# Kernel tuning notes

Hardware: AMD Instinct MI355X
Metric: run time of the kernel (lower is better)

Reference implementation:

```python
import jax, jax.numpy as jnp
import numpy as np

NH = 50000; NO = 50000; E = 500000; D = 256; L = 8; B = 512; C = 117


def setup_inputs() -> dict:
    key = jax.random.key(0)
    ks = jax.random.split(key, 32)
    s = 0.05
    inp = {
        'x_human': jax.random.normal(ks[0], (NH, D), jnp.float32),
        'x_object': jax.random.normal(ks[1], (NO, D), jnp.float32),
        'edge_index_ho': jax.random.randint(ks[2], (2, E), 0, NH),
        'edge_index_oh': jax.random.randint(ks[3], (2, E), 0, NO),
        'edge_attr_ho': jax.random.normal(ks[4], (E, 2), jnp.float32),
        'edge_attr_oh': jax.random.normal(ks[5], (E, 2), jnp.float32),
        'hbatch': jnp.sort(jax.random.randint(ks[6], (NH,), 0, B)),
        'obatch': jnp.sort(jax.random.randint(ks[7], (NO,), 0, B)),
    }
    # GATConv params per relation, stacked over L layers
    names = ['Wsrc', 'Wdst', 'asrc', 'adst', 'Wedge', 'aedge', 'bias']
    shapes = [(L, D, D), (L, D, D), (L, D), (L, D), (L, 2, D), (L, D), (L, D)]
    i = 8
    for rel in ['ho', 'oh']:
        for n, sh in zip(names, shapes):
            inp[f'{n}_{rel}'] = jax.random.normal(ks[i], sh, jnp.float32) * s
            i += 1
    inp['W_emlp'] = jax.random.normal(ks[i], (2, 32), jnp.float32) * s
    inp['b_emlp'] = jnp.zeros((32,), jnp.float32)
    inp['W_p1'] = jax.random.normal(ks[i + 1], (2 * D + 32, C), jnp.float32) * s
    inp['b_p1'] = jnp.zeros((C,), jnp.float32)
    inp['W_p2'] = jax.random.normal(ks[i + 2], (2 * D + 32, C), jnp.float32) * s
    inp['b_p2'] = jnp.zeros((C,), jnp.float32)
    return inp


def _gat(x_src, x_dst, ei, ea, Wsrc, Wdst, asrc, adst, Wedge, aedge, bias, num_dst):
    # PyG GATConv (heads=1, edge_dim=2, add_self_loops=False)
    h_src = x_src @ Wsrc                       # [Ns, D]
    h_dst = x_dst @ Wdst                       # [Nd, D]
    src, dst = ei[0], ei[1]
    a_s = h_src @ asrc                         # [Ns]
    a_d = h_dst @ adst                         # [Nd]
    a_e = (ea @ Wedge) @ aedge                 # [E]
    logit = jax.nn.leaky_relu(a_s[src] + a_d[dst] + a_e, 0.2)
    m = jax.ops.segment_max(logit, dst, num_segments=num_dst)
    ex = jnp.exp(logit - m[dst])
    denom = jax.ops.segment_sum(ex, dst, num_segments=num_dst)
    alpha = ex / denom[dst]                    # segment softmax over dst
    out = jax.ops.segment_sum(h_src[src] * alpha[:, None], dst, num_segments=num_dst)
    return out + bias


def _seg_mean(x, seg, num):
    s = jax.ops.segment_sum(x, seg, num_segments=num)
    cnt = jax.ops.segment_sum(jnp.ones((x.shape[0],), x.dtype), seg, num_segments=num)
    return s / jnp.maximum(cnt, 1.0)[:, None]


def reference(x_human, x_object, edge_index_ho, edge_index_oh, edge_attr_ho,
              edge_attr_oh, hbatch, obatch,
              Wsrc_ho, Wdst_ho, asrc_ho, adst_ho, Wedge_ho, aedge_ho, bias_ho,
              Wsrc_oh, Wdst_oh, asrc_oh, adst_oh, Wedge_oh, aedge_oh, bias_oh,
              W_emlp, b_emlp, W_p1, b_p1, W_p2, b_p2):
    xh, xo = x_human, x_object
    ph, po = None, None
    for l in range(L):
        nxo = _gat(xh, xo, edge_index_ho, edge_attr_ho, Wsrc_ho[l], Wdst_ho[l],
                   asrc_ho[l], adst_ho[l], Wedge_ho[l], aedge_ho[l], bias_ho[l], NO)
        nxh = _gat(xo, xh, edge_index_oh, edge_attr_oh, Wsrc_oh[l], Wdst_oh[l],
                   asrc_oh[l], adst_oh[l], Wedge_oh[l], aedge_oh[l], bias_oh[l], NH)
        nxh = jax.nn.relu(nxh)
        nxo = jax.nn.relu(nxo)
        if ph is not None:
            nxh = nxh + ph
            nxo = nxo + po
        ph, po = nxh, nxo
        xh, xo = nxh, nxo
    hpool = _seg_mean(xh, hbatch, B)           # [B, D]
    opool = _seg_mean(xo, obatch, B)           # [B, D]
    ea = jax.nn.relu(edge_attr_ho @ W_emlp + b_emlp)  # [E, 32]
    edge_batch = hbatch[edge_index_ho[0]]
    epool = _seg_mean(ea, edge_batch, B)       # [B, 32]
    graph_emb = jnp.concatenate([hpool, opool, epool], axis=-1)  # [B, 544]
    l1 = jax.nn.softmax(graph_emb @ W_p1 + b_p1, axis=1)
    l2 = jax.nn.softmax(graph_emb @ W_p2 + b_p2, axis=1)
    return jnp.stack((l1, l2), axis=1)         # [B, 2, C]
```

## Files before the change

### kernel.cpp

```cpp
#include <hip/hip_runtime.h>
#include <math.h>


#define NNODE 50000
#define EDG   500000
#define DIM   256
#define LAY   8
#define BB    512
#define CC    117
#define EMBD  544
#define SCB   49

typedef short bf16x8 __attribute__((ext_vector_type(8)));
typedef float f32x4  __attribute__((ext_vector_type(4)));

static __device__ __forceinline__ float lrelu(float x){ return x >= 0.f ? x : 0.2f*x; }
static __device__ __forceinline__ unsigned short f2b(float f){
  unsigned int u = __float_as_uint(f);
  unsigned int r = (u + 0x7fffu + ((u >> 16) & 1u)) >> 16;
  return (unsigned short)r;
}
static __device__ __forceinline__ float b2f(unsigned short u){
  return __uint_as_float(((unsigned int)u) << 16);
}

__global__ void vcompute_k(const float* __restrict__ Wsho, const float* __restrict__ Wdho,
                           const float* __restrict__ asho, const float* __restrict__ adho,
                           const float* __restrict__ Wsoh, const float* __restrict__ Wdoh,
                           const float* __restrict__ asoh, const float* __restrict__ adoh,
                           float* __restrict__ vbuf){
  int gid = blockIdx.x*blockDim.x + threadIdx.x;
  int wv = gid >> 6, lane = gid & 63;
  if (wv >= 32*DIM) return;
  int p = wv >> 8, k = wv & 255;
  int which = p & 1, rel = (p>>1)&1, l = p>>2;
  const float* W; const float* a;
  if (rel==0){ W = which? Wdho : Wsho; a = which? adho : asho; }
  else       { W = which? Wdoh : Wsoh; a = which? adoh : asoh; }
  W += (size_t)l*DIM*DIM; a += (size_t)l*DIM;
  const float4* w4 = (const float4*)(W + (size_t)k*DIM);
  const float4* a4 = (const float4*)a;
  float4 wv4 = w4[lane], av4 = a4[lane];
  float s = wv4.x*av4.x + wv4.y*av4.y + wv4.z*av4.z + wv4.w*av4.w;
  for (int off=32; off; off>>=1) s += __shfl_xor(s, off);
  if (lane==0) vbuf[(size_t)p*DIM + k] = s;
}

__global__ void wecompute_k(const float* __restrict__ Weho, const float* __restrict__ aeho,
                            const float* __restrict__ Weoh, const float* __restrict__ aeoh,
                            float* __restrict__ webuf){
  int blk = blockIdx.x;
  int rel = blk & 1, l = blk >> 1;
  const float* We = rel? Weoh : Weho;
  const float* ae = rel? aeoh : aeho;
  int lane = threadIdx.x;
  const float4* w0 = (const float4*)(We + (size_t)l*2*DIM);
  const float4* w1 = (const float4*)(We + (size_t)l*2*DIM + DIM);
  const float4* a4 = (const float4*)(ae + (size_t)l*DIM);
  float4 av = a4[lane], x0 = w0[lane], x1 = w1[lane];
  float s0 = x0.x*av.x + x0.y*av.y + x0.z*av.z + x0.w*av.w;
  float s1 = x1.x*av.x + x1.y*av.y + x1.z*av.z + x1.w*av.w;
  for (int off=32; off; off>>=1){ s0 += __shfl_xor(s0, off); s1 += __shfl_xor(s1, off); }
  if (lane==0){ webuf[blk*2] = s0; webuf[blk*2+1] = s1; }
}

__global__ void hist3_k(const int* __restrict__ ei_ho, const int* __restrict__ ei_oh,
                        int* __restrict__ cnt_ho, int* __restrict__ cnt_oh,
                        int* __restrict__ cnt_src){
  int e = blockIdx.x*blockDim.x + threadIdx.x;
  if (e >= EDG) return;
  int y = blockIdx.y;
  if (y == 0)      atomicAdd(&cnt_ho[ei_ho[EDG + e]], 1);
  else if (y == 1) atomicAdd(&cnt_oh[ei_oh[EDG + e]], 1);
  else             atomicAdd(&cnt_src[ei_ho[e]], 1);
}

__global__ void scanA_k(const int* __restrict__ c0, const int* __restrict__ c1,
                        const int* __restrict__ c2, int* __restrict__ bsum){
  __shared__ int sh[256];
  int y = blockIdx.y, b = blockIdx.x, t = threadIdx.x;
  const int* cnt = (y==0)? c0 : (y==1)? c1 : c2;
  int idx = b*1024 + t*4;
  int s = 0;
  if (idx + 3 < NNODE){
    int4 v = *(const int4*)(cnt + idx);
    s = v.x + v.y + v.z + v.w;
  } else {
    for (int j=0;j<4;j++) if (idx+j < NNODE) s += cnt[idx+j];
  }
  sh[t] = s; __syncthreads();
  for (int off=128; off; off>>=1){ if (t<off) sh[t] += sh[t+off]; __syncthreads(); }
  if (t==0) bsum[y*SCB + b] = sh[0];
}

__global__ void scanB_k(int* __restrict__ bsum, int* __restrict__ boff,
                        int* __restrict__ rp0, int* __restrict__ rp1, int* __restrict__ rp2){
  int t = threadIdx.x;
  if (t >= 3) return;
  int run = 0;
  for (int i=0;i<SCB;i++){ boff[t*SCB+i] = run; run += bsum[t*SCB+i]; }
  int* rp = (t==0)? rp0 : (t==1)? rp1 : rp2;
  rp[NNODE] = run;
}

__global__ void scanC_k(const int* __restrict__ c0, const int* __restrict__ c1,
                        const int* __restrict__ c2, const int* __restrict__ boff,
                        int* __restrict__ rp0, int* __restrict__ rp1, int* __restrict__ rp2){
  __shared__ int sh[256];
  int y = blockIdx.y, b = blockIdx.x, t = threadIdx.x;
  const int* cnt = (y==0)? c0 : (y==1)? c1 : c2;
  int* rp = (y==0)? rp0 : (y==1)? rp1 : rp2;
  int idx = b*1024 + t*4;
  int c[4] = {0,0,0,0};
  if (idx + 3 < NNODE){
    int4 v = *(const int4*)(cnt + idx);
    c[0]=v.x; c[1]=v.y; c[2]=v.z; c[3]=v.w;
  } else {
    for (int j=0;j<4;j++) if (idx+j < NNODE) c[j] = cnt[idx+j];
  }
  int mysum = c[0]+c[1]+c[2]+c[3];
  sh[t] = mysum; __syncthreads();
  for (int off=1; off<256; off<<=1){
    int v = (t>=off) ? sh[t-off] : 0;
    __syncthreads();
    sh[t] += v;
    __syncthreads();
  }
  int base = boff[y*SCB + b] + (sh[t] - mysum);
  int run = 0;
  for (int j=0;j<4;j++){
    if (idx+j < NNODE) rp[idx+j] = base + run;
    run += c[j];
  }
}

__global__ void scatter_k(const int* __restrict__ ei, const float* __restrict__ ea,
                          const int* __restrict__ rowptr, int* __restrict__ cursor,
                          int* __restrict__ srcs, float2* __restrict__ eaperm){
  int e = blockIdx.x*blockDim.x + threadIdx.x;
  if (e >= EDG) return;
  int d = ei[EDG + e];
  int pos = rowptr[d] + atomicAdd(&cursor[d], 1);
  srcs[pos] = ei[e];
  eaperm[pos] = make_float2(ea[2*e], ea[2*e+1]);
}

__global__ void scatter_src_k(const int* __restrict__ ei, const float* __restrict__ ea,
                              const int* __restrict__ rowptr, int* __restrict__ cursor,
                              float2* __restrict__ eaperm){
  int e = blockIdx.x*blockDim.x + threadIdx.x;
  if (e >= EDG) return;
  int s = ei[e];
  int pos = rowptr[s] + atomicAdd(&cursor[s], 1);
  eaperm[pos] = make_float2(ea[2*e], ea[2*e+1]);
}

__global__ void xconv_k(const float* __restrict__ in, unsigned short* __restrict__ out, int n4){
  int i = blockIdx.x*blockDim.x + threadIdx.x;
  if (i >= n4) return;
  float4 v = ((const float4*)in)[i];
  ushort4 o; o.x=f2b(v.x); o.y=f2b(v.y); o.z=f2b(v.z); o.w=f2b(v.w);
  ((ushort4*)out)[i] = o;
}

__global__ void wtconv_k(const float* __restrict__ Who, const float* __restrict__ Woh,
                         unsigned short* __restrict__ Wt){
  int gid = blockIdx.x*blockDim.x + threadIdx.x;
  int rel = gid >> 19;
  int rem = gid & ((1<<19)-1);
  int l = rem >> 16;
  int idx = rem & 65535;
  int n = idx >> 8, k = idx & 255;
  const float* W = rel ? Woh : Who;
  Wt[gid] = f2b(W[(size_t)l*65536 + (size_t)k*256 + n]);
}

__global__ __launch_bounds__(256) void gemmb_k(const unsigned short* __restrict__ A,
                                               const unsigned short* __restrict__ Bt,
                                               unsigned short* __restrict__ H, int M){
  __shared__ __align__(16) unsigned short As[4096];
  __shared__ __align__(16) unsigned short Bs[4096];
  int tid = threadIdx.x;
  int col0 = blockIdx.x * 128;
  int row0 = blockIdx.y * 128;
  int w = tid >> 6, lane = tid & 63;
  int q = lane >> 4, ml = lane & 15;
  f32x4 acc[2][8];
  #pragma unroll
  for (int i=0;i<2;i++)
    #pragma unroll
    for (int j=0;j<8;j++) acc[i][j] = (f32x4){0.f,0.f,0.f,0.f};
  int srow = tid >> 2;
  int sq   = tid & 3;
  for (int k0 = 0; k0 < 256; k0 += 32){
    #pragma unroll
    for (int p = 0; p < 2; ++p){
      int row = p*64 + srow;
      int gr = row0 + row;
      uint4 av = make_uint4(0,0,0,0);
      if (gr < M) av = *(const uint4*)(A + (size_t)gr*256 + k0 + sq*8);
      *(uint4*)&As[((((row>>4)*4) + sq)*16 + (row&15))*8] = av;
      int gc = col0 + row;
      uint4 bv = *(const uint4*)(Bt + (size_t)gc*256 + k0 + sq*8);
      *(uint4*)&Bs[((((row>>4)*4) + sq)*16 + (row&15))*8] = bv;
    }
    __syncthreads();
    bf16x8 a0 = *(const bf16x8*)&As[(((2*w+0)*4 + q)*16 + ml)*8];
    bf16x8 a1 = *(const bf16x8*)&As[(((2*w+1)*4 + q)*16 + ml)*8];
    #pragma unroll
    for (int nf = 0; nf < 8; ++nf){
      bf16x8 b = *(const bf16x8*)&Bs[((nf*4 + q)*16 + ml)*8];
      acc[0][nf] = __builtin_amdgcn_mfma_f32_16x16x32_bf16(a0, b, acc[0][nf], 0,0,0);
      acc[1][nf] = __builtin_amdgcn_mfma_f32_16x16x32_bf16(a1, b, acc[1][nf], 0,0,0);
    }
    __syncthreads();
  }
  #pragma unroll
  for (int mf = 0; mf < 2; ++mf){
    #pragma unroll
    for (int r = 0; r < 4; ++r){
      int gr = row0 + 32*w + 16*mf + q*4 + r;
      if (gr < M){
        #pragma unroll
        for (int nf = 0; nf < 8; ++nf)
          H[(size_t)gr*256 + col0 + nf*16 + ml] = f2b(acc[mf][nf][r]);
      }
    }
  }
}

__global__ void dgemv_k(const float* __restrict__ X, const float* __restrict__ v1,
                        const float* __restrict__ v2, float* __restrict__ o1,
                        float* __restrict__ o2){
  int gid = blockIdx.x*blockDim.x + threadIdx.x;
  int w = gid >> 6, lane = gid & 63;
  if (w >= NNODE) return;
  const float4* x4 = (const float4*)(X + (size_t)w*DIM);
  float4 xv = x4[lane];
  float4 a = ((const float4*)v1)[lane];
  float4 b = ((const float4*)v2)[lane];
  float s1 = xv.x*a.x + xv.y*a.y + xv.z*a.z + xv.w*a.w;
  float s2 = xv.x*b.x + xv.y*b.y + xv.z*b.z + xv.w*b.w;
  for (int off=32; off; off>>=1){ s1 += __shfl_xor(s1, off); s2 += __shfl_xor(s2, off); }
  if (lane==0){ o1[w] = s1; o2[w] = s2; }
}

__global__ void attn_k(const int* __restrict__ rowptr, const int* __restrict__ srcs,
                       const float2* __restrict__ eaperm, const float* __restrict__ a_s,
                       const float* __restrict__ a_d,
                       const float* __restrict__ wep, const unsigned short* __restrict__ hs,
                       const float* __restrict__ bias, const unsigned short* __restrict__ xprev,
                       unsigned short* __restrict__ xnext,
                       const float* __restrict__ vsn, const float* __restrict__ vdn,
                       float* __restrict__ asn, float* __restrict__ adn,
                       int hasRes, int doNext){
  int gid = blockIdx.x*blockDim.x + threadIdx.x;
  int w = gid >> 6, lane = gid & 63;
  if (w >= NNODE) return;
  int st = rowptr[w], en = rowptr[w+1];
  int deg = en - st;
  float w0 = wep[0], w1 = wep[1];
  float adv = a_d[w];
  float ax=0.f, ay=0.f, az=0.f, aw=0.f;
  const ushort4* h4 = (const ushort4*)hs;
  if (deg > 0 && deg <= 64){
    int sreg = 0; float lg = -INFINITY;
    if (lane < deg){
      sreg = srcs[st + lane];
      float2 ev = eaperm[st + lane];
      lg = lrelu(a_s[sreg] + adv + ev.x*w0 + ev.y*w1);
    }
    float mx = lg;
    for (int off=32; off; off>>=1) mx = fmaxf(mx, __shfl_xor(mx, off));
    float ex = (lane < deg) ? expf(lg - mx) : 0.f;
    float sm = ex;
    for (int off=32; off; off>>=1) sm += __shfl_xor(sm, off);
    float wgt = ex / sm;
    int i = 0;
    for (; i + 3 < deg; i += 4){
      float wi0 = __shfl(wgt, i),   wi1 = __shfl(wgt, i+1);
      float wi2 = __shfl(wgt, i+2), wi3 = __shfl(wgt, i+3);
      int   si0 = __shfl(sreg, i),   si1 = __shfl(sreg, i+1);
      int   si2 = __shfl(sreg, i+2), si3 = __shfl(sreg, i+3);
      ushort4 h0 = h4[(size_t)si0*64 + lane];
      ushort4 h1 = h4[(size_t)si1*64 + lane];
      ushort4 h2 = h4[(size_t)si2*64 + lane];
      ushort4 h3 = h4[(size_t)si3*64 + lane];
      ax += wi0*b2f(h0.x) + wi1*b2f(h1.x) + wi2*b2f(h2.x) + wi3*b2f(h3.x);
      ay += wi0*b2f(h0.y) + wi1*b2f(h1.y) + wi2*b2f(h2.y) + wi3*b2f(h3.y);
      az += wi0*b2f(h0.z) + wi1*b2f(h1.z) + wi2*b2f(h2.z) + wi3*b2f(h3.z);
      aw += wi0*b2f(h0.w) + wi1*b2f(h1.w) + wi2*b2f(h2.w) + wi3*b2f(h3.w);
    }
    for (; i < deg; ++i){
      float wi = __shfl(wgt, i);
      int   si = __shfl(sreg, i);
      ushort4 hv = h4[(size_t)si*64 + lane];
      ax += wi*b2f(hv.x); ay += wi*b2f(hv.y); az += wi*b2f(hv.z); aw += wi*b2f(hv.w);
    }
  } else if (deg > 64){
    float mx = -INFINITY;
    for (int p = st + lane; p < en; p += 64){
      float2 ev = eaperm[p];
      float lg = lrelu(a_s[srcs[p]] + adv + ev.x*w0 + ev.y*w1);
      mx = fmaxf(mx, lg);
    }
    for (int off=32; off; off>>=1) mx = fmaxf(mx, __shfl_xor(mx, off));
    float sm = 0.f;
    for (int p = st + lane; p < en; p += 64){
      float2 ev = eaperm[p];
      float lg = lrelu(a_s[srcs[p]] + adv + ev.x*w0 + ev.y*w1);
      sm += expf(lg - mx);
    }
    for (int off=32; off; off>>=1) sm += __shfl_xor(sm, off);
    float inv = 1.f/sm;
    for (int p = st; p < en; ++p){
      float2 ev = eaperm[p];
      int s = srcs[p];
      float lg = lrelu(a_s[s] + adv + ev.x*w0 + ev.y*w1);
      float wgt = expf(lg - mx) * inv;
      ushort4 hv = h4[(size_t)s*64 + lane];
      ax += wgt*b2f(hv.x); ay += wgt*b2f(hv.y); az += wgt*b2f(hv.z); aw += wgt*b2f(hv.w);
    }
  }
  float4 bv = ((const float4*)bias)[lane];
  float4 o;
  o.x = fmaxf(ax + bv.x, 0.f);
  o.y = fmaxf(ay + bv.y, 0.f);
  o.z = fmaxf(az + bv.z, 0.f);
  o.w = fmaxf(aw + bv.w, 0.f);
  if (hasRes){
    ushort4 r = ((const ushort4*)xprev)[(size_t)w*64 + lane];
    o.x += b2f(r.x); o.y += b2f(r.y); o.z += b2f(r.z); o.w += b2f(r.w);
  }
  ushort4 ob; ob.x=f2b(o.x); ob.y=f2b(o.y); ob.z=f2b(o.z); ob.w=f2b(o.w);
  ((ushort4*)xnext)[(size_t)w*64 + lane] = ob;
  if (doNext){
    float4 a = ((const float4*)vsn)[lane];
    float4 b = ((const float4*)vdn)[lane];
    float s1 = o.x*a.x + o.y*a.y + o.z*a.z + o.w*a.w;
    float s2 = o.x*b.x + o.y*b.y + o.z*b.z + o.w*b.w;
    for (int off=32; off; off>>=1){ s1 += __shfl_xor(s1, off); s2 += __shfl_xor(s2, off); }
    if (lane==0){ asn[w] = s1; adn[w] = s2; }
  }
}

__device__ __forceinline__ int lowerb(const int* a, int n, int v){
  int lo=0, hi=n;
  while (lo < hi){ int m = (lo+hi)>>1; if (a[m] < v) lo = m+1; else hi = m; }
  return lo;
}

__global__ void pool_k(const unsigned short* __restrict__ x, const int* __restrict__ batch,
                       float* __restrict__ out){
  int b = blockIdx.x, t = threadIdx.x;
  int st = lowerb(batch, NNODE, b), en = lowerb(batch, NNODE, b+1);
  float s = 0.f;
  for (int i=st;i<en;i++) s += b2f(x[(size_t)i*DIM + t]);
  out[(size_t)b*DIM + t] = s / fmaxf((float)(en - st), 1.f);
}

__global__ void epool_k(const int* __restrict__ rp_src, const int* __restrict__ hbatch,
                        const float2* __restrict__ eaperm, const float* __restrict__ Wem,
                        const float* __restrict__ bem, float* __restrict__ epool){
  __shared__ float ps[8][33];
  int b = blockIdx.x, t = threadIdx.x;
  int j = t & 31, g = t >> 5;
  int nst = lowerb(hbatch, NNODE, b), nen = lowerb(hbatch, NNODE, b+1);
  int est = rp_src[nst], een = rp_src[nen];
  float w0 = Wem[j], w1 = Wem[32+j], bb = bem[j];
  float s = 0.f;
  for (int p = est + g; p < een; p += 8){
    float2 e = eaperm[p];
    s += fmaxf(e.x*w0 + e.y*w1 + bb, 0.f);
  }
  ps[g][j] = s; __syncthreads();
  if (g == 0){
    float tot = 0.f;
    #pragma unroll
    for (int gg=0; gg<8; gg++) tot += ps[gg][j];
    epool[(size_t)b*32 + j] = tot / fmaxf((float)(een - est), 1.f);
  }
}

__global__ void head_k(const float* __restrict__ hpool, const float* __restrict__ opool,
                       const float* __restrict__ epool,
                       const float* __restrict__ Wp1, const float* __restrict__ bp1,
                       const float* __restrict__ Wp2, const float* __restrict__ bp2,
                       float* __restrict__ out){
  __shared__ float emb[EMBD];
  __shared__ float red[256];
  int b = blockIdx.x, t = threadIdx.x;
  emb[t] = hpool[(size_t)b*DIM + t];
  emb[DIM + t] = opool[(size_t)b*DIM + t];
  if (t < 32) emb[2*DIM + t] = epool[(size_t)b*32 + t];
  __syncthreads();
  for (int h = 0; h < 2; ++h){
    const float* Wp = h? Wp2 : Wp1;
    const float* bp = h? bp2 : bp1;
    float logit = -INFINITY;
    if (t < CC){
      float s = bp[t];
      for (int k=0;k<EMBD;k++) s += emb[k]*Wp[(size_t)k*CC + t];
      logit = s;
    }
    red[t] = logit; __syncthreads();
    for (int off=128; off; off>>=1){ if (t<off) red[t] = fmaxf(red[t], red[t+off]); __syncthreads(); }
    float mx = red[0]; __syncthreads();
    float ex = (t < CC) ? expf(logit - mx) : 0.f;
    red[t] = ex; __syncthreads();
    for (int off=128; off; off>>=1){ if (t<off) red[t] += red[t+off]; __syncthreads(); }
    float sm = red[0]; __syncthreads();
    if (t < CC) out[((size_t)b*2 + h)*CC + t] = ex / sm;
  }
}

extern "C" void kernel_launch(void* const* d_in, const int* in_sizes, int n_in,
                              void* d_out, int out_size, void* d_ws, size_t ws_size,
                              hipStream_t stream) {
  (void)in_sizes; (void)n_in; (void)out_size; (void)ws_size;
  const float* xh_in   = (const float*)d_in[0];
  const float* xo_in   = (const float*)d_in[1];
  const int*   ei_ho   = (const int*)d_in[2];
  const int*   ei_oh   = (const int*)d_in[3];
  const float* ea_ho   = (const float*)d_in[4];
  const float* ea_oh   = (const float*)d_in[5];
  const int*   hbatch  = (const int*)d_in[6];
  const int*   obatch  = (const int*)d_in[7];
  const float* Wsrc_ho = (const float*)d_in[8];
  const float* Wdst_ho = (const float*)d_in[9];
  const float* asrc_ho = (const float*)d_in[10];
  const float* adst_ho = (const float*)d_in[11];
  const float* Wedge_ho= (const float*)d_in[12];
  const float* aedge_ho= (const float*)d_in[13];
  const float* bias_ho = (const float*)d_in[14];
  const float* Wsrc_oh = (const float*)d_in[15];
  const float* Wdst_oh = (const float*)d_in[16];
  const float* asrc_oh = (const float*)d_in[17];
  const float* adst_oh = (const float*)d_in[18];
  const float* Wedge_oh= (const float*)d_in[19];
  const float* aedge_oh= (const float*)d_in[20];
  const float* bias_oh = (const float*)d_in[21];
  const float* W_emlp  = (const float*)d_in[22];
  const float* b_emlp  = (const float*)d_in[23];
  const float* W_p1    = (const float*)d_in[24];
  const float* b_p1    = (const float*)d_in[25];
  const float* W_p2    = (const float*)d_in[26];
  const float* b_p2    = (const float*)d_in[27];
  float* out = (float*)d_out;

  size_t ND = (size_t)NNODE*DIM;
  float* f = (float*)d_ws;
  float* aset0 = f;
  float* aset1 = aset0 + 4*NNODE;
  float* vbuf  = aset1 + 4*NNODE;
  float* webuf = vbuf + 32*DIM;
  float* hpool = webuf + 32;
  float* opool = hpool + (size_t)BB*DIM;
  float* epool = opool + (size_t)BB*DIM;
  float2* eap_ho  = (float2*)(epool + (size_t)BB*32);
  float2* eap_oh  = eap_ho + EDG;
  float2* eap_src = eap_oh + EDG;
  unsigned short* xhb_in = (unsigned short*)(eap_src + EDG);
  unsigned short* xob_in = xhb_in + ND;
  unsigned short* xhb0 = xob_in + ND;
  unsigned short* xhb1 = xhb0 + ND;
  unsigned short* xob0 = xhb1 + ND;
  unsigned short* xob1 = xob0 + ND;
  unsigned short* hSb  = xob1 + ND;
  unsigned short* Wtb  = hSb + ND;
  int* cnt_ho  = (int*)(Wtb + (size_t)2*LAY*DIM*DIM);
  int* cnt_oh  = cnt_ho + NNODE;
  int* cnt_src = cnt_oh + NNODE;
  int* rp_ho   = cnt_src + NNODE;
  int* rp_oh   = rp_ho + NNODE + 1;
  int* rp_src  = rp_oh + NNODE + 1;
  int* srcs_ho = rp_src + NNODE + 1;
  int* srcs_oh = srcs_ho + EDG;
  int* bsum    = srcs_oh + EDG;
  int* boff    = bsum + 3*SCB;

  hipMemsetAsync(cnt_ho, 0, sizeof(int)*3*NNODE, stream);
  vcompute_k<<<2048, 256, 0, stream>>>(Wsrc_ho, Wdst_ho, asrc_ho, adst_ho,
                                       Wsrc_oh, Wdst_oh, asrc_oh, adst_oh, vbuf);
  wecompute_k<<<16, 64, 0, stream>>>(Wedge_ho, aedge_ho, Wedge_oh, aedge_oh, webuf);
  wtconv_k<<<4096, 256, 0, stream>>>(Wsrc_ho, Wsrc_oh, Wtb);
  xconv_k<<<12500, 256, 0, stream>>>(xh_in, xhb_in, (int)(ND/4));
  xconv_k<<<12500, 256, 0, stream>>>(xo_in, xob_in, (int)(ND/4));
  hist3_k<<<dim3(1954,3), 256, 0, stream>>>(ei_ho, ei_oh, cnt_ho, cnt_oh, cnt_src);
  scanA_k<<<dim3(SCB,3), 256, 0, stream>>>(cnt_ho, cnt_oh, cnt_src, bsum);
  scanB_k<<<1, 64, 0, stream>>>(bsum, boff, rp_ho, rp_oh, rp_src);
  scanC_k<<<dim3(SCB,3), 256, 0, stream>>>(cnt_ho, cnt_oh, cnt_src, boff, rp_ho, rp_oh, rp_src);
  hipMemsetAsync(cnt_ho, 0, sizeof(int)*3*NNODE, stream);
  scatter_k<<<1954, 256, 0, stream>>>(ei_ho, ea_ho, rp_ho, cnt_ho, srcs_ho, eap_ho);
  scatter_k<<<1954, 256, 0, stream>>>(ei_oh, ea_oh, rp_oh, cnt_oh, srcs_oh, eap_oh);
  scatter_src_k<<<1954, 256, 0, stream>>>(ei_ho, ea_ho, rp_src, cnt_src, eap_src);

  dgemv_k<<<12500, 256, 0, stream>>>(xh_in, vbuf + (size_t)0*DIM, vbuf + (size_t)3*DIM,
                                     aset0 + 0*NNODE, aset0 + 3*NNODE);
  dgemv_k<<<12500, 256, 0, stream>>>(xo_in, vbuf + (size_t)2*DIM, vbuf + (size_t)1*DIM,
                                     aset0 + 2*NNODE, aset0 + 1*NNODE);

  const unsigned short* xh = xhb_in;
  const unsigned short* xo = xob_in;
  unsigned short* xh_bufs[2] = {xhb0, xhb1};
  unsigned short* xo_bufs[2] = {xob0, xob1};
  float* asets[2] = {aset0, aset1};
  for (int l = 0; l < LAY; ++l){
    unsigned short* xo_n = xo_bufs[l & 1];
    unsigned short* xh_n = xh_bufs[l & 1];
    float* cur = asets[l & 1];
    float* nxt = asets[(l & 1) ^ 1];
    int doNext = (l < LAY-1);
    int ln = doNext ? (l+1) : l;
    gemmb_k<<<dim3(2, 391), 256, 0, stream>>>(xh, Wtb + (size_t)l*DIM*DIM, hSb, NNODE);
    attn_k<<<12500, 256, 0, stream>>>(rp_ho, srcs_ho, eap_ho,
                                      cur + 0*NNODE, cur + 1*NNODE,
                                      webuf + (size_t)(l*2+0)*2, hSb,
                                      bias_ho + (size_t)l*DIM, xo, xo_n,
                                      vbuf + (size_t)(ln*4+2)*DIM, vbuf + (size_t)(ln*4+1)*DIM,
                                      nxt + 2*NNODE, nxt + 1*NNODE, l > 0, doNext);
    gemmb_k<<<dim3(2, 391), 256, 0, stream>>>(xo, Wtb + (size_t)(LAY + l)*DIM*DIM, hSb, NNODE);
    attn_k<<<12500, 256, 0, stream>>>(rp_oh, srcs_oh, eap_oh,
                                      cur + 2*NNODE, cur + 3*NNODE,
                                      webuf + (size_t)(l*2+1)*2, hSb,
                                      bias_oh + (size_t)l*DIM, xh, xh_n,
                                      vbuf + (size_t)(ln*4+0)*DIM, vbuf + (size_t)(ln*4+3)*DIM,
                                      nxt + 0*NNODE, nxt + 3*NNODE, l > 0, doNext);
    xh = xh_n; xo = xo_n;
  }

  pool_k<<<BB, 256, 0, stream>>>(xh, hbatch, hpool);
  pool_k<<<BB, 256, 0, stream>>>(xo, obatch, opool);
  epool_k<<<BB, 256, 0, stream>>>(rp_src, hbatch, eap_src, W_emlp, b_emlp, epool);
  head_k<<<BB, 256, 0, stream>>>(hpool, opool, epool, W_p1, b_p1, W_p2, b_p2, out);
}
```

Baseline: 1.742 ms.

## Batch both relations per launch, privatize histogram, fuse preprocessing kernels

Merges the two per-relation GEMM and attention launches into single launches indexed by a grid dimension, using separate projection buffers so both run together. The global-atomic degree histogram is replaced by shared-memory privatized partial histograms that the scan kernels sum. The three scatter kernels, the bf16 conversion and the initial dot-product kernels are fused. The attention gather loop is unrolled to eight neighbours. The aim is to cut launch count and serialization and expose more parallelism per launch, at the cost of extra partial-histogram memory traffic and higher register use.

Measured after the change: 1.560 ms. 10.4% less time.

```diff
diff --git a/kernel.cpp b/kernel.cpp
--- a/kernel.cpp
+++ b/kernel.cpp
@@ -10,6 +10,9 @@
 #define CC    117
 #define EMBD  544
 #define SCB   49
+#define HW    16384
+#define HC    16
+#define HNW   4
 
 typedef short bf16x8 __attribute__((ext_vector_type(8)));
 typedef float f32x4  __attribute__((ext_vector_type(4)));
@@ -64,29 +67,50 @@
   if (lane==0){ webuf[blk*2] = s0; webuf[blk*2+1] = s1; }
 }
 
-__global__ void hist3_k(const int* __restrict__ ei_ho, const int* __restrict__ ei_oh,
-                        int* __restrict__ cnt_ho, int* __restrict__ cnt_oh,
-                        int* __restrict__ cnt_src){
-  int e = blockIdx.x*blockDim.x + threadIdx.x;
-  if (e >= EDG) return;
-  int y = blockIdx.y;
-  if (y == 0)      atomicAdd(&cnt_ho[ei_ho[EDG + e]], 1);
-  else if (y == 1) atomicAdd(&cnt_oh[ei_oh[EDG + e]], 1);
-  else             atomicAdd(&cnt_src[ei_ho[e]], 1);
-}
-
-__global__ void scanA_k(const int* __restrict__ c0, const int* __restrict__ c1,
-                        const int* __restrict__ c2, int* __restrict__ bsum){
+__global__ void histp_k(const int* __restrict__ ei_ho, const int* __restrict__ ei_oh,
+                        int* __restrict__ phist){
+  __shared__ int h[HW];
+  int x = blockIdx.x, y = blockIdx.y, z = blockIdx.z, t = threadIdx.x;
+  for (int i=t; i<HW; i+=256) h[i] = 0;
+  __syncthreads();
+  const int* keys = (z==0)? (ei_ho + EDG) : (z==1)? (ei_oh + EDG) : ei_ho;
+  int lo = y << 14;
+  int e0 = x * (EDG/HC), e1 = e0 + (EDG/HC);
+  for (int e = e0 + t; e < e1; e += 256){
+    int k = keys[e] - lo;
+    if ((unsigned)k < (unsigned)HW) atomicAdd(&h[k], 1);
+  }
+  __syncthreads();
+  int* dst = phist + (size_t)(((z*HNW + y)*HC + x))*HW;
+  for (int i=t; i<HW; i+=256) dst[i] = h[i];
+}
+
+static __device__ __forceinline__ int4 phist_sum4(const int* __restrict__ phist,
+                                                  int z, int idx){
+  int win = idx >> 14, off = idx & (HW-1);
+  const int* base = phist + (size_t)((z*HNW + win)*HC)*HW + off;
+  int4 s = make_int4(0,0,0,0);
+  #pragma unroll
+  for (int c=0;c<HC;c++){
+    int4 v = *(const int4*)(base + (size_t)c*HW);
+    s.x += v.x; s.y += v.y; s.z += v.z; s.w += v.w;
+  }
+  return s;
+}
+
+__global__ void scanA_k(const int* __restrict__ phist, int* __restrict__ bsum){
   __shared__ int sh[256];
   int y = blockIdx.y, b = blockIdx.x, t = threadIdx.x;
-  const int* cnt = (y==0)? c0 : (y==1)? c1 : c2;
   int idx = b*1024 + t*4;
   int s = 0;
   if (idx + 3 < NNODE){
-    int4 v = *(const int4*)(cnt + idx);
+    int4 v = phist_sum4(phist, y, idx);
     s = v.x + v.y + v.z + v.w;
   } else {
-    for (int j=0;j<4;j++) if (idx+j < NNODE) s += cnt[idx+j];
+    for (int j=0;j<4;j++) if (idx+j < NNODE){
+      int win = (idx+j) >> 14, off = (idx+j) & (HW-1);
+      for (int c=0;c<HC;c++) s += phist[(size_t)((y*HNW+win)*HC+c)*HW + off];
+    }
   }
   sh[t] = s; __syncthreads();
   for (int off=128; off; off>>=1){ if (t<off) sh[t] += sh[t+off]; __syncthreads(); }
@@ -103,20 +127,21 @@
   rp[NNODE] = run;
 }
 
-__global__ void scanC_k(const int* __restrict__ c0, const int* __restrict__ c1,
-                        const int* __restrict__ c2, const int* __restrict__ boff,
+__global__ void scanC_k(const int* __restrict__ phist, const int* __restrict__ boff,
                         int* __restrict__ rp0, int* __restrict__ rp1, int* __restrict__ rp2){
   __shared__ int sh[256];
   int y = blockIdx.y, b = blockIdx.x, t = threadIdx.x;
-  const int* cnt = (y==0)? c0 : (y==1)? c1 : c2;
   int* rp = (y==0)? rp0 : (y==1)? rp1 : rp2;
   int idx = b*1024 + t*4;
   int c[4] = {0,0,0,0};
   if (idx + 3 < NNODE){
-    int4 v = *(const int4*)(cnt + idx);
+    int4 v = phist_sum4(phist, y, idx);
     c[0]=v.x; c[1]=v.y; c[2]=v.z; c[3]=v.w;
   } else {
-    for (int j=0;j<4;j++) if (idx+j < NNODE) c[j] = cnt[idx+j];
+    for (int j=0;j<4;j++) if (idx+j < NNODE){
+      int win = (idx+j) >> 14, off = (idx+j) & (HW-1);
+      for (int cc=0;cc<HC;cc++) c[j] += phist[(size_t)((y*HNW+win)*HC+cc)*HW + off];
+    }
   }
   int mysum = c[0]+c[1]+c[2]+c[3];
   sh[t] = mysum; __syncthreads();
@@ -134,33 +159,55 @@
   }
 }
 
-__global__ void scatter_k(const int* __restrict__ ei, const float* __restrict__ ea,
-                          const int* __restrict__ rowptr, int* __restrict__ cursor,
-                          int* __restrict__ srcs, float2* __restrict__ eaperm){
+__global__ void scatter3_k(const int* __restrict__ ei_ho, const int* __restrict__ ei_oh,
+                           const float* __restrict__ ea_ho, const float* __restrict__ ea_oh,
+                           const int* __restrict__ rp0, const int* __restrict__ rp1,
+                           const int* __restrict__ rp2, int* __restrict__ cur,
+                           int* __restrict__ srcs0, int* __restrict__ srcs1,
+                           float2* __restrict__ eap0, float2* __restrict__ eap1,
+                           float2* __restrict__ eap2){
   int e = blockIdx.x*blockDim.x + threadIdx.x;
   if (e >= EDG) return;
-  int d = ei[EDG + e];
-  int pos = rowptr[d] + atomicAdd(&cursor[d], 1);
-  srcs[pos] = ei[e];
-  eaperm[pos] = make_float2(ea[2*e], ea[2*e+1]);
-}
-
-__global__ void scatter_src_k(const int* __restrict__ ei, const float* __restrict__ ea,
-                              const int* __restrict__ rowptr, int* __restrict__ cursor,
-                              float2* __restrict__ eaperm){
-  int e = blockIdx.x*blockDim.x + threadIdx.x;
-  if (e >= EDG) return;
-  int s = ei[e];
-  int pos = rowptr[s] + atomicAdd(&cursor[s], 1);
-  eaperm[pos] = make_float2(ea[2*e], ea[2*e+1]);
-}
-
-__global__ void xconv_k(const float* __restrict__ in, unsigned short* __restrict__ out, int n4){
-  int i = blockIdx.x*blockDim.x + threadIdx.x;
-  if (i >= n4) return;
-  float4 v = ((const float4*)in)[i];
-  ushort4 o; o.x=f2b(v.x); o.y=f2b(v.y); o.z=f2b(v.z); o.w=f2b(v.w);
-  ((ushort4*)out)[i] = o;
+  int y = blockIdx.y;
+  if (y == 0){
+    int d = ei_ho[EDG + e];
+    int pos = rp0[d] + atomicAdd(&cur[d], 1);
+    srcs0[pos] = ei_ho[e];
+    eap0[pos] = make_float2(ea_ho[2*e], ea_ho[2*e+1]);
+  } else if (y == 1){
+    int d = ei_oh[EDG + e];
+    int pos = rp1[d] + atomicAdd(&cur[NNODE + d], 1);
+    srcs1[pos] = ei_oh[e];
+    eap1[pos] = make_float2(ea_oh[2*e], ea_oh[2*e+1]);
+  } else {
+    int s = ei_ho[e];
+    int pos = rp2[s] + atomicAdd(&cur[2*NNODE + s], 1);
+    eap2[pos] = make_float2(ea_ho[2*e], ea_ho[2*e+1]);
+  }
+}
+
+__global__ void xcdg_k(const float* __restrict__ xh_in, const float* __restrict__ xo_in,
+                       unsigned short* __restrict__ xhb, unsigned short* __restrict__ xob,
+                       const float* __restrict__ vbuf, float* __restrict__ aset){
+  int gid = blockIdx.x*blockDim.x + threadIdx.x;
+  int w = gid >> 6, lane = gid & 63;
+  if (w >= NNODE) return;
+  int z = blockIdx.y;
+  const float* X = z? xo_in : xh_in;
+  unsigned short* O = z? xob : xhb;
+  const float* v1 = vbuf + (size_t)(z? 2:0)*DIM;
+  const float* v2 = vbuf + (size_t)(z? 1:3)*DIM;
+  float* o1 = aset + (size_t)(z? 2:0)*NNODE;
+  float* o2 = aset + (size_t)(z? 1:3)*NNODE;
+  float4 xv = ((const float4*)(X + (size_t)w*DIM))[lane];
+  ushort4 ob; ob.x=f2b(xv.x); ob.y=f2b(xv.y); ob.z=f2b(xv.z); ob.w=f2b(xv.w);
+  ((ushort4*)O)[(size_t)w*64 + lane] = ob;
+  float4 a = ((const float4*)v1)[lane];
+  float4 b = ((const float4*)v2)[lane];
+  float s1 = xv.x*a.x + xv.y*a.y + xv.z*a.z + xv.w*a.w;
+  float s2 = xv.x*b.x + xv.y*b.y + xv.z*b.z + xv.w*b.w;
+  for (int off=32; off; off>>=1){ s1 += __shfl_xor(s1, off); s2 += __shfl_xor(s2, off); }
+  if (lane==0){ o1[w] = s1; o2[w] = s2; }
 }
 
 __global__ void wtconv_k(const float* __restrict__ Who, const float* __restrict__ Woh,
@@ -175,11 +222,18 @@
   Wt[gid] = f2b(W[(size_t)l*65536 + (size_t)k*256 + n]);
 }
 
-__global__ __launch_bounds__(256) void gemmb_k(const unsigned short* __restrict__ A,
-                                               const unsigned short* __restrict__ Bt,
-                                               unsigned short* __restrict__ H, int M){
+__global__ __launch_bounds__(256) void gemmb2_k(const unsigned short* __restrict__ A0,
+                                                const unsigned short* __restrict__ A1,
+                                                const unsigned short* __restrict__ B0,
+                                                const unsigned short* __restrict__ B1,
+                                                unsigned short* __restrict__ H0,
+                                                unsigned short* __restrict__ H1, int M){
   __shared__ __align__(16) unsigned short As[4096];
   __shared__ __align__(16) unsigned short Bs[4096];
+  int z = blockIdx.z;
+  const unsigned short* A  = z? A1 : A0;
+  const unsigned short* Bt = z? B1 : B0;
+  unsigned short* H        = z? H1 : H0;
   int tid = threadIdx.x;
   int col0 = blockIdx.x * 128;
   int row0 = blockIdx.y * 128;
@@ -229,37 +283,38 @@
   }
 }
 
-__global__ void dgemv_k(const float* __restrict__ X, const float* __restrict__ v1,
-                        const float* __restrict__ v2, float* __restrict__ o1,
-                        float* __restrict__ o2){
+__global__ void attn2_k(const int* __restrict__ rp0, const int* __restrict__ srcs0,
+                        const float2* __restrict__ eap0,
+                        const int* __restrict__ rp1, const int* __restrict__ srcs1,
+                        const float2* __restrict__ eap1,
+                        const float* __restrict__ cur_a, float* __restrict__ nxt_a,
+                        const float* __restrict__ wepl,
+                        const unsigned short* __restrict__ hs0,
+                        const unsigned short* __restrict__ hs1,
+                        const float* __restrict__ bias0, const float* __restrict__ bias1,
+                        const unsigned short* __restrict__ xprev0,
+                        const unsigned short* __restrict__ xprev1,
+                        unsigned short* __restrict__ xnext0,
+                        unsigned short* __restrict__ xnext1,
+                        const float* __restrict__ vbl,
+                        int hasRes, int doNext){
   int gid = blockIdx.x*blockDim.x + threadIdx.x;
   int w = gid >> 6, lane = gid & 63;
   if (w >= NNODE) return;
-  const float4* x4 = (const float4*)(X + (size_t)w*DIM);
-  float4 xv = x4[lane];
-  float4 a = ((const float4*)v1)[lane];
-  float4 b = ((const float4*)v2)[lane];
-  float s1 = xv.x*a.x + xv.y*a.y + xv.z*a.z + xv.w*a.w;
-  float s2 = xv.x*b.x + xv.y*b.y + xv.z*b.z + xv.w*b.w;
-  for (int off=32; off; off>>=1){ s1 += __shfl_xor(s1, off); s2 += __shfl_xor(s2, off); }
-  if (lane==0){ o1[w] = s1; o2[w] = s2; }
-}
-
-__global__ void attn_k(const int* __restrict__ rowptr, const int* __restrict__ srcs,
-                       const float2* __restrict__ eaperm, const float* __restrict__ a_s,
-                       const float* __restrict__ a_d,
-                       const float* __restrict__ wep, const unsigned short* __restrict__ hs,
-                       const float* __restrict__ bias, const unsigned short* __restrict__ xprev,
-                       unsigned short* __restrict__ xnext,
-                       const float* __restrict__ vsn, const float* __restrict__ vdn,
-                       float* __restrict__ asn, float* __restrict__ adn,
-                       int hasRes, int doNext){
-  int gid = blockIdx.x*blockDim.x + threadIdx.x;
-  int w = gid >> 6, lane = gid & 63;
-  if (w >= NNODE) return;
+  int rel = blockIdx.y;
+  const int* rowptr = rel? rp1 : rp0;
+  const int* srcs   = rel? srcs1 : srcs0;
+  const float2* eaperm = rel? eap1 : eap0;
+  const float* a_s = cur_a + (size_t)(rel? 2:0)*NNODE;
+  const float* a_d = cur_a + (size_t)(rel? 3:1)*NNODE;
+  float w0 = wepl[rel? 2:0], w1 = wepl[rel? 3:1];
+  const unsigned short* hs = rel? hs1 : hs0;
+  const float* bias = rel? bias1 : bias0;
+  const unsigned short* xprev = rel? xprev1 : xprev0;
+  unsigned short* xnext = rel? xnext1 : xnext0;
+
   int st = rowptr[w], en = rowptr[w+1];
   int deg = en - st;
-  float w0 = wep[0], w1 = wep[1];
   float adv = a_d[w];
   float ax=0.f, ay=0.f, az=0.f, aw=0.f;
   const ushort4* h4 = (const ushort4*)hs;
@@ -277,19 +332,31 @@
     for (int off=32; off; off>>=1) sm += __shfl_xor(sm, off);
     float wgt = ex / sm;
     int i = 0;
+    for (; i + 7 < deg; i += 8){
+      float wi[8]; int si[8];
+      #pragma unroll
+      for (int j=0;j<8;j++){ wi[j] = __shfl(wgt, i+j); si[j] = __shfl(sreg, i+j); }
+      ushort4 hv[8];
+      #pragma unroll
+      for (int j=0;j<8;j++) hv[j] = h4[(size_t)si[j]*64 + lane];
+      #pragma unroll
+      for (int j=0;j<8;j++){
+        ax += wi[j]*b2f(hv[j].x); ay += wi[j]*b2f(hv[j].y);
+        az += wi[j]*b2f(hv[j].z); aw += wi[j]*b2f(hv[j].w);
+      }
+    }
     for (; i + 3 < deg; i += 4){
-      float wi0 = __shfl(wgt, i),   wi1 = __shfl(wgt, i+1);
-      float wi2 = __shfl(wgt, i+2), wi3 = __shfl(wgt, i+3);
-      int   si0 = __shfl(sreg, i),   si1 = __shfl(sreg, i+1);
-      int   si2 = __shfl(sreg, i+2), si3 = __shfl(sreg, i+3);
-      ushort4 h0 = h4[(size_t)si0*64 + lane];
-      ushort4 h1 = h4[(size_t)si1*64 + lane];
-      ushort4 h2 = h4[(size_t)si2*64 + lane];
-      ushort4 h3 = h4[(size_t)si3*64 + lane];
-      ax += wi0*b2f(h0.x) + wi1*b2f(h1.x) + wi2*b2f(h2.x) + wi3*b2f(h3.x);
-      ay += wi0*b2f(h0.y) + wi1*b2f(h1.y) + wi2*b2f(h2.y) + wi3*b2f(h3.y);
-      az += wi0*b2f(h0.z) + wi1*b2f(h1.z) + wi2*b2f(h2.z) + wi3*b2f(h3.z);
-      aw += wi0*b2f(h0.w) + wi1*b2f(h1.w) + wi2*b2f(h2.w) + wi3*b2f(h3.w);
+      float wi[4]; int si[4];
+      #pragma unroll
+      for (int j=0;j<4;j++){ wi[j] = __shfl(wgt, i+j); si[j] = __shfl(sreg, i+j); }
+      ushort4 hv[4];
+      #pragma unroll
+      for (int j=0;j<4;j++) hv[j] = h4[(size_t)si[j]*64 + lane];
+      #pragma unroll
+      for (int j=0;j<4;j++){
+        ax += wi[j]*b2f(hv[j].x); ay += wi[j]*b2f(hv[j].y);
+        az += wi[j]*b2f(hv[j].z); aw += wi[j]*b2f(hv[j].w);
+      }
     }
     for (; i < deg; ++i){
       float wi = __shfl(wgt, i);
@@ -335,6 +402,10 @@
   ushort4 ob; ob.x=f2b(o.x); ob.y=f2b(o.y); ob.z=f2b(o.z); ob.w=f2b(o.w);
   ((ushort4*)xnext)[(size_t)w*64 + lane] = ob;
   if (doNext){
+    const float* vsn = vbl + (size_t)(rel? 0:2)*DIM;
+    const float* vdn = vbl + (size_t)(rel? 3:1)*DIM;
+    float* asn = nxt_a + (size_t)(rel? 0:2)*NNODE;
+    float* adn = nxt_a + (size_t)(rel? 3:1)*NNODE;
     float4 a = ((const float4*)vsn)[lane];
     float4 b = ((const float4*)vdn)[lane];
     float s1 = o.x*a.x + o.y*a.y + o.z*a.z + o.w*a.w;
@@ -350,8 +421,13 @@
   return lo;
 }
 
-__global__ void pool_k(const unsigned short* __restrict__ x, const int* __restrict__ batch,
-                       float* __restrict__ out){
+__global__ void pool2_k(const unsigned short* __restrict__ xh, const unsigned short* __restrict__ xo,
+                        const int* __restrict__ hbatch, const int* __restrict__ obatch,
+                        float* __restrict__ hpool, float* __restrict__ opool){
+  int z = blockIdx.y;
+  const unsigned short* x = z? xo : xh;
+  const int* batch = z? obatch : hbatch;
+  float* out = z? opool : hpool;
   int b = blockIdx.x, t = threadIdx.x;
   int st = lowerb(batch, NNODE, b), en = lowerb(batch, NNODE, b+1);
   float s = 0.f;
@@ -460,77 +536,66 @@
   float2* eap_ho  = (float2*)(epool + (size_t)BB*32);
   float2* eap_oh  = eap_ho + EDG;
   float2* eap_src = eap_oh + EDG;
-  unsigned short* xhb_in = (unsigned short*)(eap_src + EDG);
-  unsigned short* xob_in = xhb_in + ND;
-  unsigned short* xhb0 = xob_in + ND;
+  unsigned short* xhb0 = (unsigned short*)(eap_src + EDG);
   unsigned short* xhb1 = xhb0 + ND;
   unsigned short* xob0 = xhb1 + ND;
   unsigned short* xob1 = xob0 + ND;
-  unsigned short* hSb  = xob1 + ND;
-  unsigned short* Wtb  = hSb + ND;
-  int* cnt_ho  = (int*)(Wtb + (size_t)2*LAY*DIM*DIM);
-  int* cnt_oh  = cnt_ho + NNODE;
-  int* cnt_src = cnt_oh + NNODE;
-  int* rp_ho   = cnt_src + NNODE;
+  unsigned short* hSb0 = xob1 + ND;
+  unsigned short* hSb1 = hSb0 + ND;
+  unsigned short* Wtb  = hSb1 + ND;
+  int* cur     = (int*)(Wtb + (size_t)2*LAY*DIM*DIM);
+  int* rp_ho   = cur + 3*NNODE;
   int* rp_oh   = rp_ho + NNODE + 1;
   int* rp_src  = rp_oh + NNODE + 1;
   int* srcs_ho = rp_src + NNODE + 1;
   int* srcs_oh = srcs_ho + EDG;
   int* bsum    = srcs_oh + EDG;
   int* boff    = bsum + 3*SCB;
-
-  hipMemsetAsync(cnt_ho, 0, sizeof(int)*3*NNODE, stream);
+  int* phist   = boff + 3*SCB;
+
+  hipMemsetAsync(cur, 0, sizeof(int)*3*NNODE, stream);
   vcompute_k<<<2048, 256, 0, stream>>>(Wsrc_ho, Wdst_ho, asrc_ho, adst_ho,
                                        Wsrc_oh, Wdst_oh, asrc_oh, adst_oh, vbuf);
   wecompute_k<<<16, 64, 0, stream>>>(Wedge_ho, aedge_ho, Wedge_oh, aedge_oh, webuf);
   wtconv_k<<<4096, 256, 0, stream>>>(Wsrc_ho, Wsrc_oh, Wtb);
-  xconv_k<<<12500, 256, 0, stream>>>(xh_in, xhb_in, (int)(ND/4));
-  xconv_k<<<12500, 256, 0, stream>>>(xo_in, xob_in, (int)(ND/4));
-  hist3_k<<<dim3(1954,3), 256, 0, stream>>>(ei_ho, ei_oh, cnt_ho, cnt_oh, cnt_src);
-  scanA_k<<<dim3(SCB,3), 256, 0, stream>>>(cnt_ho, cnt_oh, cnt_src, bsum);
+  histp_k<<<dim3(HC, HNW, 3), 256, 0, stream>>>(ei_ho, ei_oh, phist);
+  scanA_k<<<dim3(SCB, 3), 256, 0, stream>>>(phist, bsum);
   scanB_k<<<1, 64, 0, stream>>>(bsum, boff, rp_ho, rp_oh, rp_src);
-  scanC_k<<<dim3(SCB,3), 256, 0, stream>>>(cnt_ho, cnt_oh, cnt_src, boff, rp_ho, rp_oh, rp_src);
-  hipMemsetAsync(cnt_ho, 0, sizeof(int)*3*NNODE, stream);
-  scatter_k<<<1954, 256, 0, stream>>>(ei_ho, ea_ho, rp_ho, cnt_ho, srcs_ho, eap_ho);
-  scatter_k<<<1954, 256, 0, stream>>>(ei_oh, ea_oh, rp_oh, cnt_oh, srcs_oh, eap_oh);
-  scatter_src_k<<<1954, 256, 0, stream>>>(ei_ho, ea_ho, rp_src, cnt_src, eap_src);
-
-  dgemv_k<<<12500, 256, 0, stream>>>(xh_in, vbuf + (size_t)0*DIM, vbuf + (size_t)3*DIM,
-                                     aset0 + 0*NNODE, aset0 + 3*NNODE);
-  dgemv_k<<<12500, 256, 0, stream>>>(xo_in, vbuf + (size_t)2*DIM, vbuf + (size_t)1*DIM,
-                                     aset0 + 2*NNODE, aset0 + 1*NNODE);
-
-  const unsigned short* xh = xhb_in;
-  const unsigned short* xo = xob_in;
+  scanC_k<<<dim3(SCB, 3), 256, 0, stream>>>(phist, boff, rp_ho, rp_oh, rp_src);
+  scatter3_k<<<dim3(1954, 3), 256, 0, stream>>>(ei_ho, ei_oh, ea_ho, ea_oh,
+                                                rp_ho, rp_oh, rp_src, cur,
+                                                srcs_ho, srcs_oh, eap_ho, eap_oh, eap_src);
+  xcdg_k<<<dim3(12500, 2), 256, 0, stream>>>(xh_in, xo_in, xhb1, xob1, vbuf, aset0);
+
+  const unsigned short* xh = xhb1;
+  const unsigned short* xo = xob1;
   unsigned short* xh_bufs[2] = {xhb0, xhb1};
   unsigned short* xo_bufs[2] = {xob0, xob1};
   float* asets[2] = {aset0, aset1};
   for (int l = 0; l < LAY; ++l){
     unsigned short* xo_n = xo_bufs[l & 1];
     unsigned short* xh_n = xh_bufs[l & 1];
-    float* cur = asets[l & 1];
-    float* nxt = asets[(l & 1) ^ 1];
+    float* cur_a = asets[l & 1];
+    float* nxt_a = asets[(l & 1) ^ 1];
     int doNext = (l < LAY-1);
     int ln = doNext ? (l+1) : l;
-    gemmb_k<<<dim3(2, 391), 256, 0, stream>>>(xh, Wtb + (size_t)l*DIM*DIM, hSb, NNODE);
-    attn_k<<<12500, 256, 0, stream>>>(rp_ho, srcs_ho, eap_ho,
-                                      cur + 0*NNODE, cur + 1*NNODE,
-                                      webuf + (size_t)(l*2+0)*2, hSb,
-                                      bias_ho + (size_t)l*DIM, xo, xo_n,
-                                      vbuf + (size_t)(ln*4+2)*DIM, vbuf + (size_t)(ln*4+1)*DIM,
-                                      nxt + 2*NNODE, nxt + 1*NNODE, l > 0, doNext);
-    gemmb_k<<<dim3(2, 391), 256, 0, stream>>>(xo, Wtb + (size_t)(LAY + l)*DIM*DIM, hSb, NNODE);
-    attn_k<<<12500, 256, 0, stream>>>(rp_oh, srcs_oh, eap_oh,
-                                      cur + 2*NNODE, cur + 3*NNODE,
-                                      webuf + (size_t)(l*2+1)*2, hSb,
-                                      bias_oh + (size_t)l*DIM, xh, xh_n,
-                                      vbuf + (size_t)(ln*4+0)*DIM, vbuf + (size_t)(ln*4+3)*DIM,
-                                      nxt + 0*NNODE, nxt + 3*NNODE, l > 0, doNext);
+    gemmb2_k<<<dim3(2, 391, 2), 256, 0, stream>>>(xh, xo,
+                                                  Wtb + (size_t)l*DIM*DIM,
+                                                  Wtb + (size_t)(LAY + l)*DIM*DIM,
+                                                  hSb0, hSb1, NNODE);
+    attn2_k<<<dim3(12500, 2), 256, 0, stream>>>(rp_ho, srcs_ho, eap_ho,
+                                                rp_oh, srcs_oh, eap_oh,
+                                                cur_a, nxt_a,
+                                                webuf + (size_t)l*4,
+                                                hSb0, hSb1,
+                                                bias_ho + (size_t)l*DIM, bias_oh + (size_t)l*DIM,
+                                                xo, xh, xo_n, xh_n,
+                                                vbuf + (size_t)ln*4*DIM,
+                                                l > 0, doNext);
     xh = xh_n; xo = xo_n;
   }
 
-  pool_k<<<BB, 256, 0, stream>>>(xh, hbatch, hpool);
-  pool_k<<<BB, 256, 0, stream>>>(xo, obatch, opool);
+  pool2_k<<<dim3(BB, 2), 256, 0, stream>>>(xh, xo, hbatch, obatch, hpool, opool);
   epool_k<<<BB, 256, 0, stream>>>(rp_src, hbatch, eap_src, W_emlp, b_emlp, epool);
   head_k<<<BB, 256, 0, stream>>>(hpool, opool, epool, W_p1, b_p1, W_p2, b_p2, out);
 }
```
